# Performance work log

Measured on AMD Instinct MI355X. Metric: run time of the kernel, lower is better.

The kernel has to match this reference:

```python
import jax, jax.numpy as jnp
import numpy as np

D_MODEL = 1024
HEADS = 16
Q_DIM = 1024
HEAD_DIM = Q_DIM // HEADS


def setup_inputs() -> dict:
    key = jax.random.key(0)
    ks = jax.random.split(key, 9)
    B, S = 2, 2048
    scale = 1.0 / np.sqrt(D_MODEL)
    inp = {
        "embeddings": jax.random.normal(ks[0], (B, S, D_MODEL), dtype=jnp.float32),
        "Wq": jax.random.normal(ks[1], (D_MODEL, Q_DIM), dtype=jnp.float32) * scale,
        "bq": jnp.zeros((Q_DIM,), dtype=jnp.float32),
        "Wk": jax.random.normal(ks[2], (D_MODEL, Q_DIM), dtype=jnp.float32) * scale,
        "bk": jnp.zeros((Q_DIM,), dtype=jnp.float32),
        "Wv": jax.random.normal(ks[3], (D_MODEL, Q_DIM), dtype=jnp.float32) * scale,
        "bv": jnp.zeros((Q_DIM,), dtype=jnp.float32),
        "Wo": jax.random.normal(ks[4], (Q_DIM, D_MODEL), dtype=jnp.float32) * scale,
        "bo": jnp.zeros((D_MODEL,), dtype=jnp.float32),
    }
    return inp


def reference(embeddings, Wq, bq, Wk, bk, Wv, bv, Wo, bo):
    B, S, _ = embeddings.shape
    # projections -> [B, H, S, Dh]
    def proj(W, b):
        x = embeddings @ W + b
        return x.reshape(B, S, HEADS, HEAD_DIM).transpose(0, 2, 1, 3)
    q = proj(Wq, bq)
    k = proj(Wk, bk)
    v = proj(Wv, bv)
    # scores scaled by sqrt(head_dim) as in source (no mask, dropout is no-op)
    scores = jnp.einsum("bhqd,bhkd->bhqk", q, k) / jnp.sqrt(
        jnp.asarray(HEAD_DIM, dtype=q.dtype)
    )
    p = jax.nn.softmax(scores, axis=-1)
    attn = jnp.einsum("bhqk,bhkd->bhqd", p, v)
    attn = attn.transpose(0, 2, 1, 3).reshape(B, S, Q_DIM)
    return attn @ Wo + bo
```

## Files before the change

### kernel.cpp

```cpp
#include <hip/hip_runtime.h>
#include <hip/hip_bf16.h>

#define BB 2
#define SS 2048
#define DMODEL 1024
#define NHEADS 16
#define DHEAD 64
#define MTOT (BB*SS)
#define NQKV 3072
#define QSCALE 0.18033688011112042f

typedef short bh8 __attribute__((ext_vector_type(8)));
typedef float fx4 __attribute__((ext_vector_type(4)));
typedef unsigned int ux2 __attribute__((ext_vector_type(2)));

__device__ __forceinline__ short f2bs(float f) {
    __hip_bfloat16 h = __float2bfloat16(f);
    return *reinterpret_cast<short*>(&h);
}

__device__ __forceinline__ unsigned pk_bf16(float a, float b) {
    __hip_bfloat162 h = __float22bfloat162_rn(make_float2(a, b));
    return *reinterpret_cast<unsigned*>(&h);
}

__device__ __forceinline__ uint4 pack32(fx4 ea, fx4 eb) {
    unsigned xa = pk_bf16(ea[0], ea[1]);
    unsigned ya = pk_bf16(ea[2], ea[3]);
    unsigned xb = pk_bf16(eb[0], eb[1]);
    unsigned yb = pk_bf16(eb[2], eb[3]);
    ux2 u   = __builtin_amdgcn_permlane32_swap(xa, xb, false, false);
    ux2 d02 = __builtin_amdgcn_permlane16_swap(u.x, u.y, false, false);
    ux2 u2  = __builtin_amdgcn_permlane32_swap(ya, yb, false, false);
    ux2 d13 = __builtin_amdgcn_permlane16_swap(u2.x, u2.y, false, false);
    uint4 r;
    r.x = d02.x; r.y = d13.x; r.z = d02.y; r.w = d13.y;
    return r;
}

__device__ __forceinline__ void gload_lds16(const short* g, short* l) {
    __builtin_amdgcn_global_load_lds(
        (const __attribute__((address_space(1))) unsigned int*)g,
        (__attribute__((address_space(3))) unsigned int*)l, 16, 0, 0);
}

__global__ __launch_bounds__(256) void prep(
        const float* __restrict__ emb, short* __restrict__ Xbf,
        const float* __restrict__ Wq, const float* __restrict__ Wk,
        const float* __restrict__ Wv, const float* __restrict__ Wo,
        short* __restrict__ Wt_qkv, short* __restrict__ Wot) {
    __shared__ float tile[64][65];
    int bid = blockIdx.x, tid = threadIdx.x;
    if (bid < 4096) {
        int i = (bid * 256 + tid) * 4;
        float4 v = *(const float4*)(emb + i);
        short4 o;
        o.x = f2bs(v.x); o.y = f2bs(v.y); o.z = f2bs(v.z); o.w = f2bs(v.w);
        *(short4*)(Xbf + i) = o;
    } else {
        int b2 = bid - 4096;
        int bx = b2 & 15, by = (b2 >> 4) & 15, z = b2 >> 8;
        const float* src = (z == 0) ? Wq : (z == 1) ? Wk : (z == 2) ? Wv : Wo;
        short* dst = (z == 3) ? Wot : (Wt_qkv + (size_t)z * 1024 * 1024);
        int n0 = bx * 64, k0 = by * 64;
        int tx = tid & 63, ty = tid >> 6;
        for (int j = 0; j < 16; j++) {
            int r = ty + j * 4;
            tile[r][tx] = src[(size_t)(k0 + r) * 1024 + n0 + tx];
        }
        __syncthreads();
        int c4 = tid & 15, rr = tid >> 4;
        #pragma unroll
        for (int pass = 0; pass < 4; pass++) {
            int r = rr + pass * 16;
            short4 o;
            o.x = f2bs(tile[c4 * 4 + 0][r]);
            o.y = f2bs(tile[c4 * 4 + 1][r]);
            o.z = f2bs(tile[c4 * 4 + 2][r]);
            o.w = f2bs(tile[c4 * 4 + 3][r]);
            *(short4*)&dst[(size_t)(n0 + r) * 1024 + k0 + c4 * 4] = o;
        }
    }
}

template<int BM, int BN, int NN, int MODE>
__global__ __launch_bounds__(256, 4) void gemm_bt_t(
        const short* __restrict__ A, const short* __restrict__ Bt,
        const float* __restrict__ bq, const float* __restrict__ bk,
        const float* __restrict__ bv, const float* __restrict__ bo,
        short* __restrict__ Qout, short* __restrict__ Kout,
        short* __restrict__ Vtout, float* __restrict__ Cout) {
    const int K = 1024;
    constexpr int ROWS = BM + BN;
    constexpr int CPW  = ROWS / 64;
    constexpr int MBK  = MTOT / BM;
    constexpr int STRIP = MBK / 8;
    constexpr int MT = BM / 32, NT = BN / 32;
    __shared__ __align__(16) short S[3][ROWS * 32];

    int tid = threadIdx.x;
    int w = tid >> 6, l = tid & 63, quad = l >> 4, ln = l & 15;
    int wm = w & 1, wn = w >> 1;

    int id = blockIdx.x;
    int xcd = id & 7, local = id >> 3;
    int mi = xcd * STRIP + (local % STRIP);
    int ni = local / STRIP;
    int m0 = mi * BM, n0 = ni * BN;

    const int which = (MODE == 0) ? (n0 >> 10) : 2;
    const bool swp = (MODE == 1) || (which != 2);

    const short* gsrc[CPW];
    int loff[CPW];
    #pragma unroll
    for (int j = 0; j < CPW; j++) {
        int r0 = (w * CPW + j) * 16;
        int row = r0 + (l >> 2);
        gsrc[j] = (r0 < BM ? A + (size_t)(m0 + row) * K
                           : Bt + (size_t)(n0 + row - BM) * K) + (l & 3) * 8;
        loff[j] = r0 * 32;
    }

    short *sC = &S[0][0], *sN = &S[1][0], *sN2 = &S[2][0];
    #pragma unroll
    for (int j = 0; j < CPW; j++) gload_lds16(gsrc[j], sC + loff[j]);
    #pragma unroll
    for (int j = 0; j < CPW; j++) gload_lds16(gsrc[j] + 32, sN + loff[j]);

    fx4 acc[MT][NT] = {};
    for (int it = 0; it < 32; ++it) {
        if (it < 31) {
            if constexpr (CPW == 4)
                asm volatile("s_waitcnt vmcnt(4)\n\ts_barrier" ::: "memory");
            else if constexpr (CPW == 3)
                asm volatile("s_waitcnt vmcnt(3)\n\ts_barrier" ::: "memory");
            else
                asm volatile("s_waitcnt vmcnt(2)\n\ts_barrier" ::: "memory");
        } else {
            asm volatile("s_waitcnt vmcnt(0)\n\ts_barrier" ::: "memory");
        }
        if (it < 30) {
            int k0 = (it + 2) * 32;
            #pragma unroll
            for (int j = 0; j < CPW; j++) gload_lds16(gsrc[j] + k0, sN2 + loff[j]);
        }
        bh8 af[MT], bf[NT];
        #pragma unroll
        for (int mt = 0; mt < MT; mt++)
            af[mt] = *(const bh8*)&sC[(wm * (BM / 2) + mt * 16 + ln) * 32 + quad * 8];
        #pragma unroll
        for (int nt = 0; nt < NT; nt++)
            bf[nt] = *(const bh8*)&sC[(BM + wn * (BN / 2) + nt * 16 + ln) * 32 + quad * 8];
        if (!swp) {
            #pragma unroll
            for (int mt = 0; mt < MT; mt++)
                #pragma unroll
                for (int nt = 0; nt < NT; nt++)
                    acc[mt][nt] = __builtin_amdgcn_mfma_f32_16x16x32_bf16(af[mt], bf[nt], acc[mt][nt], 0, 0, 0);
        } else {
            #pragma unroll
            for (int mt = 0; mt < MT; mt++)
                #pragma unroll
                for (int nt = 0; nt < NT; nt++)
                    acc[mt][nt] = __builtin_amdgcn_mfma_f32_16x16x32_bf16(bf[nt], af[mt], acc[mt][nt], 0, 0, 0);
        }
        short* t;
        t = sC; sC = sN; sN = sN2; sN2 = t;
    }

    if constexpr (MODE == 0) {
        int nbase = n0 + wn * 64;
        int nn0 = nbase & 1023;
        int h = nn0 >> 6;
        int mbase_w = m0 + wm * 64;
        int bb_ = mbase_w >> 11, s0 = mbase_w & 2047;

        if (which == 2) {
            #pragma unroll
            for (int nt = 0; nt < NT; nt++) {
                float bias = bv[nn0 + nt * 16 + ln];
                fx4 bb4 = {bias, bias, bias, bias};
                int d = nt * 16 + ln;
                short* vrow = Vtout + ((size_t)(bb_ * 16 + h) * 64 + d) * 2048 + s0;
                #pragma unroll
                for (int mp = 0; mp < MT / 2; mp++) {
                    uint4 pk = pack32(acc[2 * mp][nt] + bb4, acc[2 * mp + 1][nt] + bb4);
                    *(uint4*)(vrow + (mp * 32 + quad * 8)) = pk;
                }
            }
        } else {
            const float* bptr = (which == 0) ? bq : bk;
            float scl = (which == 0) ? QSCALE : 1.0f;
            short* out = (which == 0) ? Qout : Kout;
            #pragma unroll
            for (int mt = 0; mt < MT; mt++) {
                int s_ = s0 + mt * 16 + ln;
                short* crow = out + (((size_t)(bb_ * 16 + h) * 2048) + s_) * 64;
                #pragma unroll
                for (int np = 0; np < NT / 2; np++) {
                    fx4 ba = *(const fx4*)&bptr[nn0 + (2 * np) * 16 + quad * 4];
                    fx4 bb = *(const fx4*)&bptr[nn0 + (2 * np + 1) * 16 + quad * 4];
                    fx4 ea = acc[mt][2 * np], eb = acc[mt][2 * np + 1];
                    #pragma unroll
                    for (int r = 0; r < 4; r++) {
                        ea[r] = (ea[r] + ba[r]) * scl;
                        eb[r] = (eb[r] + bb[r]) * scl;
                    }
                    uint4 pk = pack32(ea, eb);
                    *(uint4*)(crow + (np * 32 + quad * 8)) = pk;
                }
            }
        }
    } else {
        int nbase = n0 + wn * (BN / 2);
        #pragma unroll
        for (int mt = 0; mt < MT; mt++) {
            int m = m0 + wm * (BM / 2) + mt * 16 + ln;
            #pragma unroll
            for (int nt = 0; nt < NT; nt++) {
                fx4 bo4 = *(const fx4*)&bo[nbase + nt * 16 + quad * 4];
                fx4 v = acc[mt][nt] + bo4;
                *(fx4*)&Cout[(size_t)m * 1024 + nbase + nt * 16 + quad * 4] = v;
            }
        }
    }
}

__global__ __launch_bounds__(256, 4) void flash_attn(
        const short* __restrict__ Q, const short* __restrict__ Kg,
        const short* __restrict__ Vt, short* __restrict__ Ctx) {
    __shared__ __align__(16) short SH[16384];

    int tid = threadIdx.x;
    int w = tid >> 6, l = tid & 63, quad = l >> 4, ln = l & 15;
    int wq = w & 1, wk = w >> 1;
    int id = blockIdx.x;
    int xcd = id & 7, local = id >> 3;
    int bh = xcd * 4 + (local & 3);
    int qx = local >> 2;
    int qblk = qx * 64 + wq * 32;
    int b = bh >> 4, h = bh & 15;
    const short* Qb = Q  + (size_t)bh * 2048 * 64;
    const short* Kb = Kg + (size_t)bh * 2048 * 64;
    const short* Vb = Vt + (size_t)bh * 64 * 2048;
    int swz = ln & 7;

    bh8 qf[2][2];
    #pragma unroll
    for (int qt = 0; qt < 2; qt++)
        #pragma unroll
        for (int c = 0; c < 2; c++)
            qf[qt][c] = *(const bh8*)&Qb[(size_t)(qblk + qt * 16 + ln) * 64 + c * 32 + quad * 8];

    union { short s[8]; bh8 v; } one_;
    #pragma unroll
    for (int j = 0; j < 8; j++) one_.s[j] = 0x3F80;
    bh8 onesv = one_.v;

    const short* srcK[2]; const short* srcV[2]; int dstoff[2];
    #pragma unroll
    for (int j = 0; j < 2; j++) {
        int c = w * 2 + j;
        int row = c * 8 + (l >> 3);
        int pg = (l & 7) ^ (row & 7);
        srcK[j] = Kb + row * 64 + pg * 8;
        srcV[j] = Vb + (size_t)row * 2048 + pg * 8;
        dstoff[j] = c * 512;
    }

    #pragma unroll
    for (int j = 0; j < 2; j++) {
        gload_lds16(srcK[j], SH + dstoff[j]);
        gload_lds16(srcV[j], SH + 8192 + dstoff[j]);
    }

    fx4 o[2][4] = {};
    fx4 lacc[2] = {};

    for (int it = 0; it < 32; ++it) {
        int koff = (it & 1) ? 4096 : 0;
        asm volatile("s_waitcnt vmcnt(0) lgkmcnt(0)\n\ts_barrier" ::: "memory");
        if (it < 31) {
            int noff = koff ^ 4096;
            int kg = (it + 1) * 4096, vg = (it + 1) * 64;
            #pragma unroll
            for (int j = 0; j < 2; j++) {
                gload_lds16(srcK[j] + kg, SH + noff + dstoff[j]);
                gload_lds16(srcV[j] + vg, SH + 8192 + noff + dstoff[j]);
            }
        }
        const short* ksb = SH + koff;
        const short* vsb = SH + 8192 + koff;

        bh8 kf[2][2];
        #pragma unroll
        for (int mt = 0; mt < 2; mt++) {
            int krow = (wk * 32 + mt * 16 + ln) * 64;
            kf[mt][0] = *(const bh8*)&ksb[krow + ((quad ^ swz) * 8)];
            kf[mt][1] = *(const bh8*)&ksb[krow + (((quad + 4) ^ swz) * 8)];
        }
        bh8 vf[4];
        #pragma unroll
        for (int dt = 0; dt < 4; dt++)
            vf[dt] = *(const bh8*)&vsb[(dt * 16 + ln) * 64 + (((wk * 4 + quad) ^ swz) * 8)];

        fx4 s[2][2] = {};
        __builtin_amdgcn_s_setprio(1);
        #pragma unroll
        for (int mt = 0; mt < 2; mt++)
            #pragma unroll
            for (int qt = 0; qt < 2; qt++) {
                s[qt][mt] = __builtin_amdgcn_mfma_f32_16x16x32_bf16(kf[mt][0], qf[qt][0], s[qt][mt], 0, 0, 0);
                s[qt][mt] = __builtin_amdgcn_mfma_f32_16x16x32_bf16(kf[mt][1], qf[qt][1], s[qt][mt], 0, 0, 0);
            }
        __builtin_amdgcn_s_setprio(0);

        bh8 pf[2];
        #pragma unroll
        for (int qt = 0; qt < 2; qt++) {
            fx4 e0, e1;
            #pragma unroll
            for (int r = 0; r < 4; r++) {
                e0[r] = __builtin_amdgcn_exp2f(s[qt][0][r]);
                e1[r] = __builtin_amdgcn_exp2f(s[qt][1][r]);
            }
            uint4 pk = pack32(e0, e1);
            union { uint4 u; bh8 v; } pc;
            pc.u = pk;
            pf[qt] = pc.v;
        }

        __builtin_amdgcn_s_setprio(1);
        #pragma unroll
        for (int dt = 0; dt < 4; dt++) {
            o[0][dt] = __builtin_amdgcn_mfma_f32_16x16x32_bf16(vf[dt], pf[0], o[0][dt], 0, 0, 0);
            o[1][dt] = __builtin_amdgcn_mfma_f32_16x16x32_bf16(vf[dt], pf[1], o[1][dt], 0, 0, 0);
        }
        lacc[0] = __builtin_amdgcn_mfma_f32_16x16x32_bf16(onesv, pf[0], lacc[0], 0, 0, 0);
        lacc[1] = __builtin_amdgcn_mfma_f32_16x16x32_bf16(onesv, pf[1], lacc[1], 0, 0, 0);
        __builtin_amdgcn_s_setprio(0);
    }

    asm volatile("s_waitcnt vmcnt(0) lgkmcnt(0)\n\ts_barrier" ::: "memory");

    float* R  = (float*)SH + 2176;
    float* R2 = (float*)SH + 2176 + 4096;

    if (wk == 1) {
        float* Rw = R + wq * 2048;
        #pragma unroll
        for (int qt = 0; qt < 2; qt++)
            #pragma unroll
            for (int dt = 0; dt < 4; dt++)
                *(fx4*)&Rw[(((qt * 4 + dt) * 4 + quad) * 16 + ln) * 4] = o[qt][dt];
        if (quad == 0) {
            R2[wq * 32 + 0 * 16 + ln] = lacc[0][0];
            R2[wq * 32 + 1 * 16 + ln] = lacc[1][0];
        }
    }
    asm volatile("s_waitcnt lgkmcnt(0)\n\ts_barrier" ::: "memory");

    if (wk == 0) {
        float* Rw = R + wq * 2048;
        float linv[2];
        #pragma unroll
        for (int qt = 0; qt < 2; qt++) {
            #pragma unroll
            for (int dt = 0; dt < 4; dt++)
                o[qt][dt] += *(const fx4*)&Rw[(((qt * 4 + dt) * 4 + quad) * 16 + ln) * 4];
            float lf = lacc[qt][0] + R2[wq * 32 + qt * 16 + ln];
            linv[qt] = 1.0f / lf;
        }
        float* PsF = (float*)SH + wq * 1088;
        int row = l >> 2, seg = l & 3;
        #pragma unroll
        for (int qt = 0; qt < 2; qt++) {
            #pragma unroll
            for (int dt = 0; dt < 4; dt++)
                *(fx4*)&PsF[ln * 68 + dt * 16 + quad * 4] = o[qt][dt];
            asm volatile("s_waitcnt lgkmcnt(0)" ::: "memory");
            float invr = __shfl(linv[qt], row);
            int q = qblk + qt * 16 + row;
            short* crow = Ctx + ((size_t)(b * 2048 + q)) * 1024 + h * 64 + seg * 16;
            union { short s[8]; uint4 u; } o0, o1;
            #pragma unroll
            for (int j = 0; j < 2; j++) {
                fx4 v = *(const fx4*)&PsF[row * 68 + seg * 16 + j * 4];
                o0.s[j * 4 + 0] = f2bs(v[0] * invr);
                o0.s[j * 4 + 1] = f2bs(v[1] * invr);
                o0.s[j * 4 + 2] = f2bs(v[2] * invr);
                o0.s[j * 4 + 3] = f2bs(v[3] * invr);
            }
            #pragma unroll
            for (int j = 2; j < 4; j++) {
                fx4 v = *(const fx4*)&PsF[row * 68 + seg * 16 + j * 4];
                o1.s[(j - 2) * 4 + 0] = f2bs(v[0] * invr);
                o1.s[(j - 2) * 4 + 1] = f2bs(v[1] * invr);
                o1.s[(j - 2) * 4 + 2] = f2bs(v[2] * invr);
                o1.s[(j - 2) * 4 + 3] = f2bs(v[3] * invr);
            }
            *(uint4*)&crow[0] = o0.u;
            *(uint4*)&crow[8] = o1.u;
            asm volatile("s_waitcnt lgkmcnt(0)" ::: "memory");
        }
    }
}

extern "C" void kernel_launch(void* const* d_in, const int* in_sizes, int n_in,
                              void* d_out, int out_size, void* d_ws, size_t ws_size,
                              hipStream_t stream) {
    const float* emb = (const float*)d_in[0];
    const float* Wq  = (const float*)d_in[1];
    const float* bq  = (const float*)d_in[2];
    const float* Wk  = (const float*)d_in[3];
    const float* bk  = (const float*)d_in[4];
    const float* Wv  = (const float*)d_in[5];
    const float* bv  = (const float*)d_in[6];
    const float* Wo  = (const float*)d_in[7];
    const float* bo  = (const float*)d_in[8];

    char* ws = (char*)d_ws;
    const size_t MB = 1024 * 1024;
    short* Xbf  = (short*)(ws + 0);
    short* Ctx  = (short*)(ws + 0);
    short* Wt   = (short*)(ws + 8 * MB);
    short* Wot  = (short*)(ws + 17 * MB);
    short* Qb   = (short*)(ws + 19 * MB);
    short* Kb   = (short*)(ws + 27 * MB);
    short* Vtb  = (short*)(ws + 35 * MB);

    prep<<<5120, 256, 0, stream>>>(emb, Xbf, Wq, Wk, Wv, Wo, Wt, Wot);
    gemm_bt_t<128, 128, NQKV, 0><<<768, 256, 0, stream>>>(
        Xbf, Wt, bq, bk, bv, nullptr, Qb, Kb, Vtb, nullptr);
    flash_attn<<<1024, 256, 0, stream>>>(Qb, Kb, Vtb, Ctx);
    gemm_bt_t<64, 64, DMODEL, 1><<<1024, 256, 0, stream>>>(
        Ctx, Wot, nullptr, nullptr, nullptr, bo, nullptr, nullptr, nullptr, (float*)d_out);
}
```

Measured before the change: 194.0 us.

## Software-pipeline attention loop so PV MFMAs of previous tile overlap QK

Restructures the attention inner loop into a software pipeline. The P·V and row-sum MFMAs for tile i now run in the same iteration as the QK MFMAs and exp for tile i+1, with a prologue and epilogue added. The point is to hide exp2/pack latency behind independent MFMA work and let tile loads run further ahead. In exchange it holds more registers live (vfA, vfB, pfA), which may lower occupancy.

```diff
diff --git a/kernel.cpp b/kernel.cpp
--- a/kernel.cpp
+++ b/kernel.cpp
@@ -274,24 +274,68 @@
         gload_lds16(srcK[j], SH + dstoff[j]);
         gload_lds16(srcV[j], SH + 8192 + dstoff[j]);
     }
+    #pragma unroll
+    for (int j = 0; j < 2; j++) {
+        gload_lds16(srcK[j] + 4096, SH + 4096 + dstoff[j]);
+        gload_lds16(srcV[j] + 64,   SH + 12288 + dstoff[j]);
+    }
 
     fx4 o[2][4] = {};
     fx4 lacc[2] = {};
-
-    for (int it = 0; it < 32; ++it) {
-        int koff = (it & 1) ? 4096 : 0;
+    bh8 vfA[4], pfA[2];
+
+    asm volatile("s_waitcnt vmcnt(4)\n\ts_barrier" ::: "memory");
+
+    {
+        bh8 kf[2][2];
+        #pragma unroll
+        for (int mt = 0; mt < 2; mt++) {
+            int krow = (wk * 32 + mt * 16 + ln) * 64;
+            kf[mt][0] = *(const bh8*)&SH[krow + ((quad ^ swz) * 8)];
+            kf[mt][1] = *(const bh8*)&SH[krow + (((quad + 4) ^ swz) * 8)];
+        }
+        #pragma unroll
+        for (int dt = 0; dt < 4; dt++)
+            vfA[dt] = *(const bh8*)&SH[8192 + (dt * 16 + ln) * 64 + (((wk * 4 + quad) ^ swz) * 8)];
+        fx4 s[2][2] = {};
+        __builtin_amdgcn_s_setprio(1);
+        #pragma unroll
+        for (int mt = 0; mt < 2; mt++)
+            #pragma unroll
+            for (int qt = 0; qt < 2; qt++) {
+                s[qt][mt] = __builtin_amdgcn_mfma_f32_16x16x32_bf16(kf[mt][0], qf[qt][0], s[qt][mt], 0, 0, 0);
+                s[qt][mt] = __builtin_amdgcn_mfma_f32_16x16x32_bf16(kf[mt][1], qf[qt][1], s[qt][mt], 0, 0, 0);
+            }
+        __builtin_amdgcn_s_setprio(0);
+        #pragma unroll
+        for (int qt = 0; qt < 2; qt++) {
+            fx4 e0, e1;
+            #pragma unroll
+            for (int r = 0; r < 4; r++) {
+                e0[r] = __builtin_amdgcn_exp2f(s[qt][0][r]);
+                e1[r] = __builtin_amdgcn_exp2f(s[qt][1][r]);
+            }
+            uint4 pk = pack32(e0, e1);
+            union { uint4 u; bh8 v; } pc;
+            pc.u = pk;
+            pfA[qt] = pc.v;
+        }
+    }
+
+    for (int it = 0; it < 31; ++it) {
         asm volatile("s_waitcnt vmcnt(0) lgkmcnt(0)\n\ts_barrier" ::: "memory");
-        if (it < 31) {
-            int noff = koff ^ 4096;
-            int kg = (it + 1) * 4096, vg = (it + 1) * 64;
+        if (it < 30) {
+            int noff = (it & 1) ? 4096 : 0;
+            int kg = (it + 2) * 4096, vg = (it + 2) * 64;
             #pragma unroll
             for (int j = 0; j < 2; j++) {
                 gload_lds16(srcK[j] + kg, SH + noff + dstoff[j]);
                 gload_lds16(srcV[j] + vg, SH + 8192 + noff + dstoff[j]);
             }
         }
-        const short* ksb = SH + koff;
-        const short* vsb = SH + 8192 + koff;
+        int coff = ((it + 1) & 1) ? 4096 : 0;
+        const short* ksb = SH + coff;
+        const short* vsb = SH + 8192 + coff;
 
         bh8 kf[2][2];
         #pragma unroll
@@ -300,10 +344,20 @@
             kf[mt][0] = *(const bh8*)&ksb[krow + ((quad ^ swz) * 8)];
             kf[mt][1] = *(const bh8*)&ksb[krow + (((quad + 4) ^ swz) * 8)];
         }
-        bh8 vf[4];
+        bh8 vfB[4];
         #pragma unroll
         for (int dt = 0; dt < 4; dt++)
-            vf[dt] = *(const bh8*)&vsb[(dt * 16 + ln) * 64 + (((wk * 4 + quad) ^ swz) * 8)];
+            vfB[dt] = *(const bh8*)&vsb[(dt * 16 + ln) * 64 + (((wk * 4 + quad) ^ swz) * 8)];
+
+        __builtin_amdgcn_s_setprio(1);
+        #pragma unroll
+        for (int dt = 0; dt < 4; dt++) {
+            o[0][dt] = __builtin_amdgcn_mfma_f32_16x16x32_bf16(vfA[dt], pfA[0], o[0][dt], 0, 0, 0);
+            o[1][dt] = __builtin_amdgcn_mfma_f32_16x16x32_bf16(vfA[dt], pfA[1], o[1][dt], 0, 0, 0);
+        }
+        lacc[0] = __builtin_amdgcn_mfma_f32_16x16x32_bf16(onesv, pfA[0], lacc[0], 0, 0, 0);
+        lacc[1] = __builtin_amdgcn_mfma_f32_16x16x32_bf16(onesv, pfA[1], lacc[1], 0, 0, 0);
+        __builtin_amdgcn_s_setprio(0);
 
         fx4 s[2][2] = {};
         __builtin_amdgcn_s_setprio(1);
@@ -316,7 +370,6 @@
             }
         __builtin_amdgcn_s_setprio(0);
 
-        bh8 pf[2];
         #pragma unroll
         for (int qt = 0; qt < 2; qt++) {
             fx4 e0, e1;
@@ -328,19 +381,21 @@
             uint4 pk = pack32(e0, e1);
             union { uint4 u; bh8 v; } pc;
             pc.u = pk;
-            pf[qt] = pc.v;
-        }
-
-        __builtin_amdgcn_s_setprio(1);
-        #pragma unroll
-        for (int dt = 0; dt < 4; dt++) {
-            o[0][dt] = __builtin_amdgcn_mfma_f32_16x16x32_bf16(vf[dt], pf[0], o[0][dt], 0, 0, 0);
-            o[1][dt] = __builtin_amdgcn_mfma_f32_16x16x32_bf16(vf[dt], pf[1], o[1][dt], 0, 0, 0);
-        }
-        lacc[0] = __builtin_amdgcn_mfma_f32_16x16x32_bf16(onesv, pf[0], lacc[0], 0, 0, 0);
-        lacc[1] = __builtin_amdgcn_mfma_f32_16x16x32_bf16(onesv, pf[1], lacc[1], 0, 0, 0);
-        __builtin_amdgcn_s_setprio(0);
-    }
+            pfA[qt] = pc.v;
+        }
+        #pragma unroll
+        for (int dt = 0; dt < 4; dt++) vfA[dt] = vfB[dt];
+    }
+
+    __builtin_amdgcn_s_setprio(1);
+    #pragma unroll
+    for (int dt = 0; dt < 4; dt++) {
+        o[0][dt] = __builtin_amdgcn_mfma_f32_16x16x32_bf16(vfA[dt], pfA[0], o[0][dt], 0, 0, 0);
+        o[1][dt] = __builtin_amdgcn_mfma_f32_16x16x32_bf16(vfA[dt], pfA[1], o[1][dt], 0, 0, 0);
+    }
+    lacc[0] = __builtin_amdgcn_mfma_f32_16x16x32_bf16(onesv, pfA[0], lacc[0], 0, 0, 0);
+    lacc[1] = __builtin_amdgcn_mfma_f32_16x16x32_bf16(onesv, pfA[1], lacc[1], 0, 0, 0);
+    __builtin_amdgcn_s_setprio(0);
 
     asm volatile("s_waitcnt vmcnt(0) lgkmcnt(0)\n\ts_barrier" ::: "memory");
 
```

Result: slower. 209.5 us (+8.0%).
